# Optimization experiments

Hardware: AMD Instinct MI355X
Metric: run time of the kernel (lower is better)

Reference implementation:

```python
import jax, jax.numpy as jnp
import numpy as np


def setup_inputs() -> dict:
    key = jax.random.key(0)
    k_x, k_q, k_k, k_v = jax.random.split(key, 4)
    seq_len, d_in, d_out = 4096, 1024, 1024
    x = jax.random.normal(k_x, (seq_len, d_in), dtype=jnp.float32)
    # torch nn.Linear weights are [d_out, d_in]; applied as x @ W.T
    scale = 1.0 / np.sqrt(d_in)
    Wq = jax.random.uniform(k_q, (d_out, d_in), jnp.float32, -scale, scale)
    Wk = jax.random.uniform(k_k, (d_out, d_in), jnp.float32, -scale, scale)
    Wv = jax.random.uniform(k_v, (d_out, d_in), jnp.float32, -scale, scale)
    return {"x": x, "Wq": Wq, "Wk": Wk, "Wv": Wv}


def reference(x, Wq, Wk, Wv):
    # x: [S, d_in]; Wq/Wk/Wv: [d_out, d_in]
    queries = x @ Wq.T          # [S, d_out]
    keys = x @ Wk.T             # [S, d_out]
    values = x @ Wv.T           # [S, d_out]
    d_k = keys.shape[-1]
    attn_scores = queries @ keys.T                      # [S, S]
    attn_weights = jax.nn.softmax(attn_scores / jnp.sqrt(jnp.float32(d_k)), axis=-1)
    S = attn_scores.shape[0]
    tril = jnp.tril(jnp.ones((S, S), dtype=attn_weights.dtype))
    masked = tril * attn_weights
    masked_norm = masked / jnp.sum(masked, axis=-1, keepdims=True)
    context_vec = masked_norm @ values                  # [S, d_out]
    return context_vec
```

## Files before the change

kernel.cpp:

```cpp
#include <hip/hip_runtime.h>
#include <hip/hip_bf16.h>


typedef __bf16 bf16_t;
typedef __bf16 bf16x4v __attribute__((ext_vector_type(4)));
typedef __bf16 bf16x8 __attribute__((ext_vector_type(8)));
typedef float f32x4 __attribute__((ext_vector_type(4)));
typedef unsigned char u8;
typedef long long i64_t;

#define AS1 __attribute__((address_space(1)))
#define AS3 __attribute__((address_space(3)))
#define WAIT_VMCNT(N) asm volatile("s_waitcnt vmcnt(" #N ")" ::: "memory")
#define BARRIER_RAW() asm volatile("s_barrier" ::: "memory")

__device__ __forceinline__ void async_copy16(const void* g, void* l) {
    __builtin_amdgcn_global_load_lds((AS1 void*)(g), (AS3 void*)(l), 16, 0, 0);
}

__device__ __forceinline__ u8 f32_to_fp8(float v) {
    return (u8)(__builtin_amdgcn_cvt_pk_fp8_f32(v, v, 0, false) & 0xff);
}

__device__ __forceinline__ void store_conv(float* p, float v) { *p = v; }
__device__ __forceinline__ void store_conv(bf16_t* p, float v) { *p = (bf16_t)v; }
__device__ __forceinline__ void store_conv(u8* p, float v) { *p = f32_to_fp8(v); }

__device__ __forceinline__ float sum32(const float* p) {
    const f32x4* v = (const f32x4*)p;
    float s = 0.f;
#pragma unroll
    for (int u = 0; u < 8; ++u) {
        f32x4 a = v[u];
        s += a[0] + a[1] + a[2] + a[3];
    }
    return s;
}

template <int EPI, typename OutT>
__device__ __forceinline__ void gemm_tile_bf16(const bf16_t* __restrict__ A, int lda,
                                               const bf16_t* __restrict__ B, int ldb,
                                               OutT* __restrict__ C, int ldc,
                                               int kb0, int kb1, float alpha,
                                               char* __restrict__ smem,
                                               const float* __restrict__ inv) {
    constexpr int BK = 64;
    bf16_t* As = (bf16_t*)smem;
    bf16_t* Bs = (bf16_t*)(smem + 32768);
    const int tid = threadIdx.x;
    const int lane = tid & 63, wave = tid >> 6;
    const int wm = wave >> 1, wn = wave & 1;
    const int q = lane >> 4, l16 = lane & 15;

    f32x4 acc[4][4] = {};

    const bf16_t* aSrc[4];
    const bf16_t* bSrc[4];
    int ldsOff[4];
#pragma unroll
    for (int it = 0; it < 4; ++it) {
        int c = it * 256 + tid;
        int r = c >> 3, b = c & 7;
        int sb = b ^ (r & 7);
        aSrc[it] = A + (size_t)r * lda + sb * 8;
        bSrc[it] = B + (size_t)r * ldb + sb * 8;
        ldsOff[it] = c * 8;
    }

    {
        const int k0 = kb0 * BK;
#pragma unroll
        for (int it = 0; it < 4; ++it) async_copy16(aSrc[it] + k0, &As[ldsOff[it]]);
#pragma unroll
        for (int it = 0; it < 4; ++it) async_copy16(bSrc[it] + k0, &Bs[ldsOff[it]]);
    }

    int cur = 0;
    for (int kb = kb0; kb < kb1; ++kb) {
        if (kb + 1 < kb1) {
            const int k0 = (kb + 1) * BK;
            const int boff = (cur ^ 1) * 8192;
#pragma unroll
            for (int it = 0; it < 4; ++it) async_copy16(aSrc[it] + k0, &As[boff + ldsOff[it]]);
#pragma unroll
            for (int it = 0; it < 4; ++it) async_copy16(bSrc[it] + k0, &Bs[boff + ldsOff[it]]);
            WAIT_VMCNT(8);
        } else {
            WAIT_VMCNT(0);
        }
        __builtin_amdgcn_sched_barrier(0);
        BARRIER_RAW();
        const bf16_t* Ab = As + cur * 8192;
        const bf16_t* Bb = Bs + cur * 8192;
        __builtin_amdgcn_s_setprio(1);
#pragma unroll
        for (int k2 = 0; k2 < 2; ++k2) {
            bf16x8 af[4], bfr[4];
#pragma unroll
            for (int mt = 0; mt < 4; ++mt) {
                int m = wm * 64 + mt * 16 + l16;
                int blk = (k2 * 4 + q) ^ (m & 7);
                af[mt] = *(const bf16x8*)&Ab[m * BK + blk * 8];
            }
#pragma unroll
            for (int nt = 0; nt < 4; ++nt) {
                int nn = wn * 64 + nt * 16 + l16;
                int blk = (k2 * 4 + q) ^ (nn & 7);
                bfr[nt] = *(const bf16x8*)&Bb[nn * BK + blk * 8];
            }
#pragma unroll
            for (int mt = 0; mt < 4; ++mt)
#pragma unroll
                for (int nt = 0; nt < 4; ++nt)
                    acc[mt][nt] = __builtin_amdgcn_mfma_f32_16x16x32_bf16(
                        af[mt], bfr[nt], acc[mt][nt], 0, 0, 0);
        }
        __builtin_amdgcn_s_setprio(0);
        BARRIER_RAW();
        cur ^= 1;
    }

    constexpr int S = (int)sizeof(OutT);
    constexpr int RB = 128 * S;
    const int row0 = wm * 64, col0 = wn * 64;
#pragma unroll
    for (int mt = 0; mt < 4; ++mt)
#pragma unroll
        for (int nt = 0; nt < 4; ++nt)
#pragma unroll
            for (int r = 0; r < 4; ++r) {
                int lr = row0 + mt * 16 + q * 4 + r;
                int lc = col0 + nt * 16 + l16;
                float v = acc[mt][nt][r];
                v = (EPI == 2) ? v * inv[lr] : v * alpha;
                int cb = (lc * S) >> 4;
                int sw = cb ^ ((lr >> 2) & 7);
                store_conv((OutT*)(smem + lr * RB + (sw << 4) + ((lc * S) & 15)), v);
            }
    __syncthreads();
#pragma unroll
    for (int p = 0; p < 4 * S; ++p) {
        int g = p * 4096 + tid * 16;
        int r = g / RB;
        int wb = g & (RB - 1);
        int sc = (wb >> 4) ^ ((r >> 2) & 7);
        f32x4 val = *(const f32x4*)(smem + r * RB + (sc << 4));
        *(f32x4*)((char*)C + (size_t)r * ((size_t)ldc * S) + wb) = val;
    }
}

__device__ __forceinline__ void scores_tile_fp8(const u8* __restrict__ A, int lda,
                                                const u8* __restrict__ B, int ldb,
                                                bf16_t* __restrict__ C, int ldc,
                                                float alpha, char* __restrict__ smem,
                                                float* __restrict__ partial,
                                                int gr0, int gc0) {
    u8* As = (u8*)smem;
    u8* Bs = (u8*)(smem + 32768);
    const int tid = threadIdx.x;
    const int lane = tid & 63, wave = tid >> 6;
    const int wm = wave >> 1, wn = wave & 1;
    const int q = lane >> 4, l16 = lane & 15;

    f32x4 acc[4][4] = {};

    const u8* aSrc[4];
    const u8* bSrc[4];
    int ldsOff[4];
#pragma unroll
    for (int it = 0; it < 4; ++it) {
        int c = it * 256 + tid;
        int r = c >> 3, b = c & 7;
        int sb = b ^ (r & 7);
        aSrc[it] = A + (size_t)r * lda + sb * 16;
        bSrc[it] = B + (size_t)r * ldb + sb * 16;
        ldsOff[it] = c * 16;
    }

    {
#pragma unroll
        for (int it = 0; it < 4; ++it) async_copy16(aSrc[it], &As[ldsOff[it]]);
#pragma unroll
        for (int it = 0; it < 4; ++it) async_copy16(bSrc[it], &Bs[ldsOff[it]]);
    }

    int cur = 0;
    for (int kb = 0; kb < 8; ++kb) {
        if (kb < 7) {
            const int k0 = (kb + 1) * 128;
            const int boff = (cur ^ 1) * 16384;
#pragma unroll
            for (int it = 0; it < 4; ++it) async_copy16(aSrc[it] + k0, &As[boff + ldsOff[it]]);
#pragma unroll
            for (int it = 0; it < 4; ++it) async_copy16(bSrc[it] + k0, &Bs[boff + ldsOff[it]]);
            WAIT_VMCNT(8);
        } else {
            WAIT_VMCNT(0);
        }
        __builtin_amdgcn_sched_barrier(0);
        BARRIER_RAW();
        const u8* Ab = As + cur * 16384;
        const u8* Bb = Bs + cur * 16384;
        __builtin_amdgcn_s_setprio(1);
#pragma unroll
        for (int k2 = 0; k2 < 4; ++k2) {
            i64_t af[4], bfr[4];
            const int cb = 2 * k2 + (q >> 1), co = (q & 1) * 8;
#pragma unroll
            for (int mt = 0; mt < 4; ++mt) {
                int m = wm * 64 + mt * 16 + l16;
                af[mt] = *(const i64_t*)&Ab[m * 128 + ((cb ^ (m & 7)) << 4) + co];
            }
#pragma unroll
            for (int nt = 0; nt < 4; ++nt) {
                int nn = wn * 64 + nt * 16 + l16;
                bfr[nt] = *(const i64_t*)&Bb[nn * 128 + ((cb ^ (nn & 7)) << 4) + co];
            }
#pragma unroll
            for (int mt = 0; mt < 4; ++mt)
#pragma unroll
                for (int nt = 0; nt < 4; ++nt)
                    acc[mt][nt] = __builtin_amdgcn_mfma_f32_16x16x32_fp8_fp8(
                        af[mt], bfr[nt], acc[mt][nt], 0, 0, 0);
        }
        __builtin_amdgcn_s_setprio(0);
        BARRIER_RAW();
        cur ^= 1;
    }

    float* sred = (float*)(smem + 32768);
    const int row0 = wm * 64, col0 = wn * 64;
    float esum[4][4];
#pragma unroll
    for (int mt = 0; mt < 4; ++mt)
#pragma unroll
        for (int r = 0; r < 4; ++r) esum[mt][r] = 0.f;
#pragma unroll
    for (int mt = 0; mt < 4; ++mt)
#pragma unroll
        for (int nt = 0; nt < 4; ++nt)
#pragma unroll
            for (int r = 0; r < 4; ++r) {
                int lr = row0 + mt * 16 + q * 4 + r;
                int lc = col0 + nt * 16 + l16;
                float pe = (gc0 + lc > gr0 + lr) ? 0.f : __expf(acc[mt][nt][r] * alpha);
                esum[mt][r] += pe;
                int sw = (lc >> 3) ^ ((lr >> 2) & 7);
                *(bf16_t*)(smem + lr * 256 + (sw << 4) + ((lc * 2) & 15)) = (bf16_t)pe;
            }
#pragma unroll
    for (int mt = 0; mt < 4; ++mt)
#pragma unroll
        for (int r = 0; r < 4; ++r) {
#pragma unroll
            for (int off = 1; off < 16; off <<= 1)
                esum[mt][r] += __shfl_xor(esum[mt][r], off, 64);
            if (l16 == 0) sred[(row0 + mt * 16 + q * 4 + r) * 2 + wn] = esum[mt][r];
        }
    __syncthreads();
#pragma unroll
    for (int p = 0; p < 8; ++p) {
        int g = p * 4096 + tid * 16;
        int r = g >> 8;
        int wb = g & 255;
        int sc = (wb >> 4) ^ ((r >> 2) & 7);
        f32x4 val = *(const f32x4*)(smem + r * 256 + (sc << 4));
        *(f32x4*)((char*)C + (size_t)r * ((size_t)ldc * 2) + wb) = val;
    }
    if (tid < 128) partial[(size_t)tid * 32] = sred[tid * 2] + sred[tid * 2 + 1];
}

__global__ __launch_bounds__(256) void k_qkv(const bf16_t* __restrict__ xb,
                                             const bf16_t* __restrict__ wqk,
                                             u8* __restrict__ qk) {
    __shared__ __attribute__((aligned(16))) char smem[65536];
    int b = blockIdx.x;
    int bm = b & 31, bn = b >> 5;
    gemm_tile_bf16<0, u8>(xb + (size_t)bm * 128 * 1024, 1024,
                          wqk + (size_t)bn * 128 * 1024, 1024,
                          qk + (size_t)bm * 128 * 2048 + bn * 128, 2048,
                          0, 16, 1.f, smem, nullptr);
}

__global__ __launch_bounds__(256) void k_sv(const bf16_t* __restrict__ xb,
                                            const bf16_t* __restrict__ wvb,
                                            const u8* __restrict__ qk,
                                            bf16_t* __restrict__ vt,
                                            bf16_t* __restrict__ P,
                                            float* __restrict__ rowsum_part) {
    __shared__ __attribute__((aligned(16))) char smem[65536];
    int b = blockIdx.x;
    if (b < 256) {
        int bm = b & 7, bn = b >> 3;
        gemm_tile_bf16<0, bf16_t>(wvb + (size_t)bm * 128 * 1024, 1024,
                                  xb + (size_t)bn * 128 * 1024, 1024,
                                  vt + (size_t)bm * 128 * 4096 + bn * 128, 4096,
                                  0, 16, 1.f, smem, nullptr);
        return;
    }
    int t = b - 256;
    int bm = (int)((sqrtf(8.f * (float)t + 1.f) - 1.f) * 0.5f);
    while (bm * (bm + 1) / 2 > t) --bm;
    while ((bm + 1) * (bm + 2) / 2 <= t) ++bm;
    int bn = t - bm * (bm + 1) / 2;
    scores_tile_fp8(qk + (size_t)bm * 128 * 2048, 2048,
                    qk + 1024 + (size_t)bn * 128 * 2048, 2048,
                    P + (size_t)bm * 128 * 4096 + bn * 128, 4096,
                    0.03125f, smem,
                    rowsum_part + (size_t)bm * 128 * 32 + bn,
                    bm * 128, bn * 128);
    if (bn == bm) {
        float* rp = rowsum_part + (size_t)bm * 128 * 32;
        int tid = threadIdx.x;
        for (int r = tid >> 4; r < 128; r += 16)
            for (int u = bm + 1 + (tid & 15); u < 32; u += 16)
                rp[r * 32 + u] = 0.f;
    }
}

__global__ __launch_bounds__(256) void k_pv(const bf16_t* __restrict__ P,
                                            const bf16_t* __restrict__ vt,
                                            const float* __restrict__ rowsum_part,
                                            float* __restrict__ out,
                                            float* __restrict__ partials) {
    __shared__ __attribute__((aligned(16))) char smem[65536];
    __shared__ float sInv[128];
    int b = blockIdx.x;
    int bn = b & 7, g = b >> 3;
    int bm, s, ns;
    if (g < 11)      { bm = g;                  s = 0;             ns = 1; }
    else if (g < 33) { bm = 11 + (g - 11) / 2;  s = (g - 11) % 2;  ns = 2; }
    else             { bm = 22 + (g - 33) / 3;  s = (g - 33) % 3;  ns = 3; }
    int nk = 2 * (bm + 1);
    int kb0 = s * nk / ns;
    int kb1 = (s + 1) * nk / ns;

    const bf16_t* A = P + (size_t)bm * 128 * 4096;
    const bf16_t* B = vt + (size_t)bn * 128 * 4096;
    if (ns == 1) {
        int tid = threadIdx.x;
        if (tid < 128)
            sInv[tid] = 1.f / sum32(rowsum_part + (size_t)(bm * 128 + tid) * 32);
        gemm_tile_bf16<2, float>(A, 4096, B, 4096,
                                 out + (size_t)bm * 128 * 1024 + bn * 128, 1024,
                                 kb0, kb1, 1.f, smem, sInv);
    } else {
        int cum = (bm < 22) ? (bm - 11) * 2 : 22 + (bm - 22) * 3;
        gemm_tile_bf16<0, float>(A, 4096, B, 4096,
                                 partials + ((size_t)(cum + s) * 8 + bn) * 16384, 128,
                                 kb0, kb1, 1.f, smem, nullptr);
    }
}

__global__ __launch_bounds__(256) void k_reduce(const float* __restrict__ partials,
                                                const float* __restrict__ rowsum_part,
                                                float* __restrict__ out) {
    int b = blockIdx.x;
    int t = b % 168, p = b / 168;
    int bm = 11 + t % 21, bn = t / 21;
    int ns = (bm < 22) ? 2 : 3;
    int cum = (bm < 22) ? (bm - 11) * 2 : 22 + (bm - 22) * 3;
    __shared__ float sInv[8];
    int tid = threadIdx.x;
    if (tid < 8) {
        int row = bm * 128 + p * 8 + tid;
        sInv[tid] = 1.f / sum32(rowsum_part + (size_t)row * 32);
    }
    __syncthreads();

    int idx = p * 1024 + tid * 4;
    int lr = idx >> 7, lc = idx & 127;
    float sx = 0.f, sy = 0.f, sz = 0.f, sw = 0.f;
    for (int u = 0; u < ns; ++u) {
        const float4 v = *(const float4*)(partials + ((size_t)(cum + u) * 8 + bn) * 16384 + idx);
        sx += v.x; sy += v.y; sz += v.z; sw += v.w;
    }
    float inv = sInv[lr - p * 8];
    float4 o = {sx * inv, sy * inv, sz * inv, sw * inv};
    *(float4*)(out + (size_t)(bm * 128 + lr) * 1024 + bn * 128 + lc) = o;
}

__global__ __launch_bounds__(256) void cast_to_bf16(const float* __restrict__ x,
                                                    const float* __restrict__ Wq,
                                                    const float* __restrict__ Wk,
                                                    const float* __restrict__ Wv,
                                                    bf16_t* __restrict__ xb,
                                                    bf16_t* __restrict__ wqk,
                                                    bf16_t* __restrict__ wv) {
    const int NX = (4096 * 1024) / 4;
    const int NW = (1024 * 1024) / 4;
    int idx = blockIdx.x * 256 + threadIdx.x;
    const float* src;
    bf16_t* dst;
    int off;
    if (idx < NX) {
        src = x; dst = xb; off = idx;
    } else if (idx < NX + NW) {
        src = Wq; dst = wqk; off = idx - NX;
    } else if (idx < NX + 2 * NW) {
        src = Wk; dst = wqk + (size_t)NW * 4; off = idx - NX - NW;
    } else {
        src = Wv; dst = wv; off = idx - NX - 2 * NW;
    }
    float4 f = ((const float4*)src)[off];
    bf16x4v o;
    o.x = (bf16_t)f.x; o.y = (bf16_t)f.y; o.z = (bf16_t)f.z; o.w = (bf16_t)f.w;
    *(bf16x4v*)(dst + (size_t)off * 4) = o;
}

extern "C" void kernel_launch(void* const* d_in, const int* in_sizes, int n_in,
                              void* d_out, int out_size, void* d_ws, size_t ws_size,
                              hipStream_t stream) {
    (void)in_sizes; (void)n_in; (void)out_size; (void)ws_size;
    const float* x  = (const float*)d_in[0];
    const float* Wq = (const float*)d_in[1];
    const float* Wk = (const float*)d_in[2];
    const float* Wv = (const float*)d_in[3];
    float* out = (float*)d_out;

    char* ws = (char*)d_ws;
    bf16_t* xb   = (bf16_t*)(ws + (size_t)0);
    bf16_t* wqk  = (bf16_t*)(ws + ((size_t)8 << 20));
    bf16_t* wvb  = (bf16_t*)(ws + ((size_t)12 << 20));
    u8*     qk   = (u8*)(ws + ((size_t)14 << 20));
    bf16_t* vt   = (bf16_t*)(ws + ((size_t)22 << 20));
    bf16_t* P    = (bf16_t*)(ws + ((size_t)30 << 20));
    float* rowsp = (float*)(ws + ((size_t)62 << 20));
    float* parts = (float*)(ws + ((size_t)64 << 20));

    cast_to_bf16<<<7168, 256, 0, stream>>>(x, Wq, Wk, Wv, xb, wqk, wvb);

    k_qkv<<<512, 256, 0, stream>>>(xb, wqk, qk);

    k_sv<<<784, 256, 0, stream>>>(xb, wvb, qk, vt, P, rowsp);

    k_pv<<<504, 256, 0, stream>>>(P, vt, rowsp, out, parts);
    k_reduce<<<2688, 256, 0, stream>>>(parts, rowsp, out);
}
```

Baseline: 174.8 us.

## Single-buffer k_sv tiles to shrink LDS and raise occupancy

Replaces the double-buffered bf16 V-projection GEMM and fp8 scores tile in k_sv with single-buffered versions that load each K-slice, sync, compute, then sync again. Shared memory drops from 64 KB to about 33 KB and launch bounds request 4 blocks per CU. The aim is to hide global-load latency through extra resident blocks instead of intra-block prefetching, at the cost of serializing load and compute within each block and adding barriers.

```diff
diff --git a/kernel.cpp b/kernel.cpp
--- a/kernel.cpp
+++ b/kernel.cpp
@@ -149,14 +149,101 @@
     }
 }
 
-__device__ __forceinline__ void scores_tile_fp8(const u8* __restrict__ A, int lda,
-                                                const u8* __restrict__ B, int ldb,
-                                                bf16_t* __restrict__ C, int ldc,
-                                                float alpha, char* __restrict__ smem,
-                                                float* __restrict__ partial,
-                                                int gr0, int gc0) {
+__device__ __forceinline__ void gemm_tile_bf16_sb(const bf16_t* __restrict__ A, int lda,
+                                                  const bf16_t* __restrict__ B, int ldb,
+                                                  bf16_t* __restrict__ C, int ldc,
+                                                  int kb1, char* __restrict__ smem) {
+    constexpr int BK = 64;
+    bf16_t* As = (bf16_t*)smem;
+    bf16_t* Bs = (bf16_t*)(smem + 16384);
+    const int tid = threadIdx.x;
+    const int lane = tid & 63, wave = tid >> 6;
+    const int wm = wave >> 1, wn = wave & 1;
+    const int q = lane >> 4, l16 = lane & 15;
+
+    f32x4 acc[4][4] = {};
+
+    const bf16_t* aSrc[4];
+    const bf16_t* bSrc[4];
+    int ldsOff[4];
+#pragma unroll
+    for (int it = 0; it < 4; ++it) {
+        int c = it * 256 + tid;
+        int r = c >> 3, b = c & 7;
+        int sb = b ^ (r & 7);
+        aSrc[it] = A + (size_t)r * lda + sb * 8;
+        bSrc[it] = B + (size_t)r * ldb + sb * 8;
+        ldsOff[it] = c * 8;
+    }
+
+    for (int kb = 0; kb < kb1; ++kb) {
+        const int k0 = kb * BK;
+#pragma unroll
+        for (int it = 0; it < 4; ++it) async_copy16(aSrc[it] + k0, &As[ldsOff[it]]);
+#pragma unroll
+        for (int it = 0; it < 4; ++it) async_copy16(bSrc[it] + k0, &Bs[ldsOff[it]]);
+        __syncthreads();
+        __builtin_amdgcn_s_setprio(1);
+#pragma unroll
+        for (int k2 = 0; k2 < 2; ++k2) {
+            bf16x8 af[4], bfr[4];
+#pragma unroll
+            for (int mt = 0; mt < 4; ++mt) {
+                int m = wm * 64 + mt * 16 + l16;
+                int blk = (k2 * 4 + q) ^ (m & 7);
+                af[mt] = *(const bf16x8*)&As[m * BK + blk * 8];
+            }
+#pragma unroll
+            for (int nt = 0; nt < 4; ++nt) {
+                int nn = wn * 64 + nt * 16 + l16;
+                int blk = (k2 * 4 + q) ^ (nn & 7);
+                bfr[nt] = *(const bf16x8*)&Bs[nn * BK + blk * 8];
+            }
+#pragma unroll
+            for (int mt = 0; mt < 4; ++mt)
+#pragma unroll
+                for (int nt = 0; nt < 4; ++nt)
+                    acc[mt][nt] = __builtin_amdgcn_mfma_f32_16x16x32_bf16(
+                        af[mt], bfr[nt], acc[mt][nt], 0, 0, 0);
+        }
+        __builtin_amdgcn_s_setprio(0);
+        __syncthreads();
+    }
+
+    constexpr int RB = 256;
+    const int row0 = wm * 64, col0 = wn * 64;
+#pragma unroll
+    for (int mt = 0; mt < 4; ++mt)
+#pragma unroll
+        for (int nt = 0; nt < 4; ++nt)
+#pragma unroll
+            for (int r = 0; r < 4; ++r) {
+                int lr = row0 + mt * 16 + q * 4 + r;
+                int lc = col0 + nt * 16 + l16;
+                int cb = (lc * 2) >> 4;
+                int sw = cb ^ ((lr >> 2) & 7);
+                *(bf16_t*)(smem + lr * RB + (sw << 4) + ((lc * 2) & 15)) =
+                    (bf16_t)acc[mt][nt][r];
+            }
+    __syncthreads();
+#pragma unroll
+    for (int p = 0; p < 8; ++p) {
+        int g = p * 4096 + tid * 16;
+        int r = g >> 8, wb = g & 255;
+        int sc = (wb >> 4) ^ ((r >> 2) & 7);
+        f32x4 val = *(const f32x4*)(smem + r * RB + (sc << 4));
+        *(f32x4*)((char*)C + (size_t)r * ((size_t)ldc * 2) + wb) = val;
+    }
+}
+
+__device__ __forceinline__ void scores_tile_fp8_sb(const u8* __restrict__ A, int lda,
+                                                   const u8* __restrict__ B, int ldb,
+                                                   bf16_t* __restrict__ C, int ldc,
+                                                   float alpha, char* __restrict__ smem,
+                                                   float* __restrict__ partial,
+                                                   int gr0, int gc0) {
     u8* As = (u8*)smem;
-    u8* Bs = (u8*)(smem + 32768);
+    u8* Bs = (u8*)(smem + 16384);
     const int tid = threadIdx.x;
     const int lane = tid & 63, wave = tid >> 6;
     const int wm = wave >> 1, wn = wave & 1;
@@ -177,30 +264,13 @@
         ldsOff[it] = c * 16;
     }
 
-    {
-#pragma unroll
-        for (int it = 0; it < 4; ++it) async_copy16(aSrc[it], &As[ldsOff[it]]);
-#pragma unroll
-        for (int it = 0; it < 4; ++it) async_copy16(bSrc[it], &Bs[ldsOff[it]]);
-    }
-
-    int cur = 0;
     for (int kb = 0; kb < 8; ++kb) {
-        if (kb < 7) {
-            const int k0 = (kb + 1) * 128;
-            const int boff = (cur ^ 1) * 16384;
-#pragma unroll
-            for (int it = 0; it < 4; ++it) async_copy16(aSrc[it] + k0, &As[boff + ldsOff[it]]);
-#pragma unroll
-            for (int it = 0; it < 4; ++it) async_copy16(bSrc[it] + k0, &Bs[boff + ldsOff[it]]);
-            WAIT_VMCNT(8);
-        } else {
-            WAIT_VMCNT(0);
-        }
-        __builtin_amdgcn_sched_barrier(0);
-        BARRIER_RAW();
-        const u8* Ab = As + cur * 16384;
-        const u8* Bb = Bs + cur * 16384;
+        const int k0 = kb * 128;
+#pragma unroll
+        for (int it = 0; it < 4; ++it) async_copy16(aSrc[it] + k0, &As[ldsOff[it]]);
+#pragma unroll
+        for (int it = 0; it < 4; ++it) async_copy16(bSrc[it] + k0, &Bs[ldsOff[it]]);
+        __syncthreads();
         __builtin_amdgcn_s_setprio(1);
 #pragma unroll
         for (int k2 = 0; k2 < 4; ++k2) {
@@ -209,12 +279,12 @@
 #pragma unroll
             for (int mt = 0; mt < 4; ++mt) {
                 int m = wm * 64 + mt * 16 + l16;
-                af[mt] = *(const i64_t*)&Ab[m * 128 + ((cb ^ (m & 7)) << 4) + co];
+                af[mt] = *(const i64_t*)&As[m * 128 + ((cb ^ (m & 7)) << 4) + co];
             }
 #pragma unroll
             for (int nt = 0; nt < 4; ++nt) {
                 int nn = wn * 64 + nt * 16 + l16;
-                bfr[nt] = *(const i64_t*)&Bb[nn * 128 + ((cb ^ (nn & 7)) << 4) + co];
+                bfr[nt] = *(const i64_t*)&Bs[nn * 128 + ((cb ^ (nn & 7)) << 4) + co];
             }
 #pragma unroll
             for (int mt = 0; mt < 4; ++mt)
@@ -224,8 +294,7 @@
                         af[mt], bfr[nt], acc[mt][nt], 0, 0, 0);
         }
         __builtin_amdgcn_s_setprio(0);
-        BARRIER_RAW();
-        cur ^= 1;
+        __syncthreads();
     }
 
     float* sred = (float*)(smem + 32768);
@@ -282,20 +351,20 @@
                           0, 16, 1.f, smem, nullptr);
 }
 
-__global__ __launch_bounds__(256) void k_sv(const bf16_t* __restrict__ xb,
-                                            const bf16_t* __restrict__ wvb,
-                                            const u8* __restrict__ qk,
-                                            bf16_t* __restrict__ vt,
-                                            bf16_t* __restrict__ P,
-                                            float* __restrict__ rowsum_part) {
-    __shared__ __attribute__((aligned(16))) char smem[65536];
+__global__ __launch_bounds__(256, 4) void k_sv(const bf16_t* __restrict__ xb,
+                                               const bf16_t* __restrict__ wvb,
+                                               const u8* __restrict__ qk,
+                                               bf16_t* __restrict__ vt,
+                                               bf16_t* __restrict__ P,
+                                               float* __restrict__ rowsum_part) {
+    __shared__ __attribute__((aligned(16))) char smem[33792];
     int b = blockIdx.x;
     if (b < 256) {
         int bm = b & 7, bn = b >> 3;
-        gemm_tile_bf16<0, bf16_t>(wvb + (size_t)bm * 128 * 1024, 1024,
-                                  xb + (size_t)bn * 128 * 1024, 1024,
-                                  vt + (size_t)bm * 128 * 4096 + bn * 128, 4096,
-                                  0, 16, 1.f, smem, nullptr);
+        gemm_tile_bf16_sb(wvb + (size_t)bm * 128 * 1024, 1024,
+                          xb + (size_t)bn * 128 * 1024, 1024,
+                          vt + (size_t)bm * 128 * 4096 + bn * 128, 4096,
+                          16, smem);
         return;
     }
     int t = b - 256;
@@ -303,12 +372,12 @@
     while (bm * (bm + 1) / 2 > t) --bm;
     while ((bm + 1) * (bm + 2) / 2 <= t) ++bm;
     int bn = t - bm * (bm + 1) / 2;
-    scores_tile_fp8(qk + (size_t)bm * 128 * 2048, 2048,
-                    qk + 1024 + (size_t)bn * 128 * 2048, 2048,
-                    P + (size_t)bm * 128 * 4096 + bn * 128, 4096,
-                    0.03125f, smem,
-                    rowsum_part + (size_t)bm * 128 * 32 + bn,
-                    bm * 128, bn * 128);
+    scores_tile_fp8_sb(qk + (size_t)bm * 128 * 2048, 2048,
+                       qk + 1024 + (size_t)bn * 128 * 2048, 2048,
+                       P + (size_t)bm * 128 * 4096 + bn * 128, 4096,
+                       0.03125f, smem,
+                       rowsum_part + (size_t)bm * 128 * 32 + bn,
+                       bm * 128, bn * 128);
     if (bn == bm) {
         float* rp = rowsum_part + (size_t)bm * 128 * 32;
         int tid = threadIdx.x;
```

Result: faster. 165.6 us (-5.3%).
